# Kernel optimization log

Measured on AMD Instinct MI355X. Metric: run time of the kernel, lower is better.

## Reference

```python
import jax, jax.numpy as jnp
import numpy as np

GRID = 20            # grid_size -> n1 = 400 nodes
CTX = 64             # context_size
HID = 10 * CTX       # hidden_dim per module code
BATCH = 256
K_ITERS = 100        # Dykstra iterations approximating the exact QP solve
LEAKY_SLOPE = 0.1


def _grid_incidence(g):
    """Incidence matrix of g x g grid DAG with right/down edges (SPO benchmark)."""
    n1 = g * g
    edges = []
    for i in range(g):
        for j in range(g):
            u = i * g + j
            if j + 1 < g:
                edges.append((u, u + 1))   # right
            if i + 1 < g:
                edges.append((u, u + g))   # down
    n2 = len(edges)
    A = np.zeros((n1, n2), dtype=np.float32)
    for e, (u, v) in enumerate(edges):
        A[u, e] = 1.0    # flow leaves u
        A[v, e] = -1.0   # flow enters v
    b = np.zeros(n1, dtype=np.float32)
    b[0] = 1.0           # source
    b[-1] = -1.0         # sink
    return A, b


def setup_inputs() -> dict:
    key = jax.random.key(0)
    ks = jax.random.split(key, 5)
    A_np, b_np = _grid_incidence(GRID)
    n2 = A_np.shape[1]
    d = jax.random.normal(ks[0], (BATCH, CTX), dtype=jnp.float32)
    W1 = jax.random.normal(ks[1], (CTX, HID), dtype=jnp.float32) / np.sqrt(CTX)
    b1 = jax.random.normal(ks[2], (HID,), dtype=jnp.float32) * 0.01
    W2 = jax.random.normal(ks[3], (HID, n2), dtype=jnp.float32) / np.sqrt(HID)
    b2 = jax.random.normal(ks[4], (n2,), dtype=jnp.float32) * 0.01
    return {
        "d": d, "W1": W1, "b1": b1, "W2": W2, "b2": b2,
        "A": jnp.asarray(A_np), "b_eq": jnp.asarray(b_np),
    }


def _solve_qp(w, A, b_eq):
    """Batched min_x w'x + 0.5||x||^2 s.t. Ax=b, x>=0 == proj of -w onto the
    feasible set, via Dykstra alternating projections (affine set / orthant)."""
    M = jnp.linalg.pinv(A @ A.T)  # [n1, n1]; AA' is the grid Laplacian (rank n1-1)

    def proj_affine(x):           # x: [B, n2]
        resid = x @ A.T - b_eq    # [B, n1]
        return x - (resid @ M) @ A

    y0 = -w                       # point to project
    p0 = jnp.zeros_like(w)
    q0 = jnp.zeros_like(w)

    def step(carry, _):
        y, p, q = carry
        t = y + p
        yp = proj_affine(t)
        p = t - yp
        t2 = yp + q
        y = jnp.maximum(t2, 0.0)  # projection onto x >= 0
        q = t2 - y
        return (y, p, q), None

    (y, _, _), _ = jax.lax.scan(step, (y0, p0, q0), None, length=K_ITERS)
    return y


def reference(d, W1, b1, W2, b2, A, b_eq):
    h = d @ W1 + b1
    h = jnp.where(h > 0, h, LEAKY_SLOPE * h)   # LeakyReLU(0.1)
    w = h @ W2 + b2                            # predicted edge costs [B, n2]
    return _solve_qp(w, A, b_eq)               # training-mode output: QP solution
```

## Files before the change

### kernel.cpp

```cpp
#include <hip/hip_runtime.h>
#include <math.h>

#define G 20
#define N1 400
#define N2 760
#define CTXS 64
#define HID 640
#define NB 256
#define ITERS 100
#define PI_F 3.14159265358979323846f

__device__ __forceinline__ int eR(int i, int j) { return (i < 19) ? (39 * i + 2 * j) : (741 + j); }
__device__ __forceinline__ int eD(int i, int j) { return (j < 19) ? (39 * i + 2 * j + 1) : (39 * i + 38); }

#define LOAD_ROW20(dst, base) do {                                          \
    const float4* _rp = (const float4*)(base);                              \
    float4 _r0 = _rp[0], _r1 = _rp[1], _r2 = _rp[2], _r3 = _rp[3], _r4 = _rp[4]; \
    dst[0]=_r0.x; dst[1]=_r0.y; dst[2]=_r0.z; dst[3]=_r0.w;                 \
    dst[4]=_r1.x; dst[5]=_r1.y; dst[6]=_r1.z; dst[7]=_r1.w;                 \
    dst[8]=_r2.x; dst[9]=_r2.y; dst[10]=_r2.z; dst[11]=_r2.w;               \
    dst[12]=_r3.x; dst[13]=_r3.y; dst[14]=_r3.z; dst[15]=_r3.w;             \
    dst[16]=_r4.x; dst[17]=_r4.y; dst[18]=_r4.z; dst[19]=_r4.w; } while (0)

__global__ __launch_bounds__(256, 1) void spnet_kernel(
    const float* __restrict__ dmat, const float* __restrict__ W1,
    const float* __restrict__ b1v, const float* __restrict__ W2,
    const float* __restrict__ b2v, float* __restrict__ out)
{
  const int tid = threadIdx.x;
  const int bb  = blockIdx.x;

  __shared__ __align__(16) float sdrow[CTXS];
  __shared__ __align__(16) float sh[HID];
  __shared__ __align__(16) float st0[N2];
  __shared__ __align__(16) float sc1[N1];
  __shared__ __align__(16) float sc2T[N1];
  __shared__ __align__(16) float sd1[N1];
  __shared__ __align__(16) float szz[N1];
  __shared__ __align__(16) float tRsTbuf[21][G];
  __shared__ __align__(16) float tDsT[G][G];

  for (int t = tid; t < 21 * G; t += 256) ((float*)tRsTbuf)[t] = 0.f;
  for (int t = tid; t < N1; t += 256) ((float*)tDsT)[t] = 0.f;
  if (tid < CTXS) sdrow[tid] = dmat[bb * CTXS + tid];

  const bool isC = (tid < 200);
  const int c  = tid / 10;
  const int u  = tid % 10;
  const int k0 = 2 * u;

  float VA0[10], VA1[10], VC[20], S0, S1;
  {
    const float n0 = 0.22360679774997896f, nk = 0.31622776601683794f;
#pragma unroll
    for (int i = 0; i < 10; ++i) {
      VA0[i] = ((k0 == 0) ? n0 : nk) * cosf((float)(k0 * (2 * i + 1)) * (PI_F / 40.f));
      VA1[i] = nk * cosf((float)((k0 + 1) * (2 * i + 1)) * (PI_F / 40.f));
    }
#pragma unroll
    for (int k = 0; k < 20; ++k)
      VC[k] = ((k == 0) ? n0 : nk) * cosf((float)(k * (2 * u + 1)) * (PI_F / 40.f));
    float lc = 2.f - 2.f * cosf((float)c * (PI_F / 20.f));
    float l0 = 2.f - 2.f * cosf((float)k0 * (PI_F / 20.f));
    float l1 = 2.f - 2.f * cosf((float)(k0 + 1) * (PI_F / 20.f));
    S0 = (c == 0 && k0 == 0) ? 0.f : 1.f / (lc + l0);
    S1 = 1.f / (lc + l1);
  }

  __syncthreads();

  if (tid < HID / 4) {
    float4 acc = *(const float4*)(b1v + 4 * tid);
#pragma unroll 4
    for (int k = 0; k < CTXS; k += 4) {
      float4 h4 = *(const float4*)(sdrow + k);
      const float* wb = W1 + k * HID + 4 * tid;
      float4 w0 = *(const float4*)(wb);
      float4 w1 = *(const float4*)(wb + HID);
      float4 w2 = *(const float4*)(wb + 2 * HID);
      float4 w3 = *(const float4*)(wb + 3 * HID);
      acc.x = fmaf(h4.x, w0.x, acc.x); acc.y = fmaf(h4.x, w0.y, acc.y);
      acc.z = fmaf(h4.x, w0.z, acc.z); acc.w = fmaf(h4.x, w0.w, acc.w);
      acc.x = fmaf(h4.y, w1.x, acc.x); acc.y = fmaf(h4.y, w1.y, acc.y);
      acc.z = fmaf(h4.y, w1.z, acc.z); acc.w = fmaf(h4.y, w1.w, acc.w);
      acc.x = fmaf(h4.z, w2.x, acc.x); acc.y = fmaf(h4.z, w2.y, acc.y);
      acc.z = fmaf(h4.z, w2.z, acc.z); acc.w = fmaf(h4.z, w2.w, acc.w);
      acc.x = fmaf(h4.w, w3.x, acc.x); acc.y = fmaf(h4.w, w3.y, acc.y);
      acc.z = fmaf(h4.w, w3.z, acc.z); acc.w = fmaf(h4.w, w3.w, acc.w);
    }
    acc.x = acc.x > 0.f ? acc.x : 0.1f * acc.x;
    acc.y = acc.y > 0.f ? acc.y : 0.1f * acc.y;
    acc.z = acc.z > 0.f ? acc.z : 0.1f * acc.z;
    acc.w = acc.w > 0.f ? acc.w : 0.1f * acc.w;
    *(float4*)(sh + 4 * tid) = acc;
  }
  __syncthreads();

  if (tid < N2 / 4) {
    float4 acc = *(const float4*)(b2v + 4 * tid);
#pragma unroll 2
    for (int k = 0; k < HID; k += 4) {
      float4 h4 = *(const float4*)(sh + k);
      const float* wb = W2 + k * N2 + 4 * tid;
      float4 w0 = *(const float4*)(wb);
      float4 w1 = *(const float4*)(wb + N2);
      float4 w2 = *(const float4*)(wb + 2 * N2);
      float4 w3 = *(const float4*)(wb + 3 * N2);
      acc.x = fmaf(h4.x, w0.x, acc.x); acc.y = fmaf(h4.x, w0.y, acc.y);
      acc.z = fmaf(h4.x, w0.z, acc.z); acc.w = fmaf(h4.x, w0.w, acc.w);
      acc.x = fmaf(h4.y, w1.x, acc.x); acc.y = fmaf(h4.y, w1.y, acc.y);
      acc.z = fmaf(h4.y, w1.z, acc.z); acc.w = fmaf(h4.y, w1.w, acc.w);
      acc.x = fmaf(h4.z, w2.x, acc.x); acc.y = fmaf(h4.z, w2.y, acc.y);
      acc.z = fmaf(h4.z, w2.z, acc.z); acc.w = fmaf(h4.z, w2.w, acc.w);
      acc.x = fmaf(h4.w, w3.x, acc.x); acc.y = fmaf(h4.w, w3.y, acc.y);
      acc.z = fmaf(h4.w, w3.z, acc.z); acc.w = fmaf(h4.w, w3.w, acc.w);
    }
    float4 s; s.x = -acc.x; s.y = -acc.y; s.z = -acc.z; s.w = -acc.w;
    *(float4*)(st0 + 4 * tid) = s;
  }

  const int  di = tid / 5, dj4 = (tid % 5) * 4;
  const bool dAct = (tid < 100) && (di < 19);
  float dT[4], dQ[4], dY[4];
  const int  rid = tid - 128;
  const bool isR = (rid >= 0 && rid < 100);
  const int  ri = isR ? (rid / 5) : 0, rj4 = isR ? ((rid % 5) * 4) : 0;
  float rT[4], rQ[4], rY[4];
#pragma unroll
  for (int m = 0; m < 4; ++m) { dT[m]=0.f; dQ[m]=0.f; dY[m]=0.f; rT[m]=0.f; rQ[m]=0.f; rY[m]=0.f; }

  __syncthreads();

  if (dAct) {
#pragma unroll
    for (int m = 0; m < 4; ++m) {
      dT[m] = st0[eD(di, dj4 + m)];
      tDsT[dj4 + m][di + 1] = dT[m];
    }
  }
  if (isR) {
#pragma unroll
    for (int m = 0; m < 4; ++m) {
      int j = rj4 + m;
      rT[m] = (j < 19) ? st0[eR(ri, j)] : 0.f;
      tRsTbuf[j + 1][ri] = rT[m];
    }
  }
  __syncthreads();

  for (int it = 0; it < ITERS; ++it) {
    if (isC) {
      float cur[20]; LOAD_ROW20(cur, &tRsTbuf[c + 1][0]);
      float lf_[20]; LOAD_ROW20(lf_, &tRsTbuf[c][0]);
      float dn_[20]; LOAD_ROW20(dn_, &tDsT[c][0]);
      float d_[20];
#pragma unroll
      for (int x = 0; x < 20; ++x) {
        float oD = (x < 19) ? dn_[x + 1] : 0.f;
        d_[x] = ((cur[x] + oD) - lf_[x]) - dn_[x];
      }
      if (c == 0)  d_[0]  -= 1.f;
      if (c == 19) d_[19] += 1.f;
      float a0 = 0.f, a1 = 0.f;
#pragma unroll
      for (int i = 0; i < 10; ++i) {
        float e_ = d_[i] + d_[19 - i], o_ = d_[i] - d_[19 - i];
        a0 = fmaf(VA0[i], e_, a0);
        a1 = fmaf(VA1[i], o_, a1);
      }
      sc1[k0 * G + c] = a0;
      sc1[(k0 + 1) * G + c] = a1;
    }
    __syncthreads();

    if (isC) {
      float d_[20]; LOAD_ROW20(d_, sc1 + 20 * c);
      float a0 = 0.f, a1 = 0.f;
#pragma unroll
      for (int j = 0; j < 10; ++j) {
        float e_ = d_[j] + d_[19 - j], o_ = d_[j] - d_[19 - j];
        a0 = fmaf(VA0[j], e_, a0);
        a1 = fmaf(VA1[j], o_, a1);
      }
      sc2T[k0 * G + c] = a0 * S0;
      sc2T[(k0 + 1) * G + c] = a1 * S1;
    }
    __syncthreads();

    if (isC) {
      float d_[20]; LOAD_ROW20(d_, sc2T + 20 * c);
      float E = 0.f, O = 0.f;
#pragma unroll
      for (int m = 0; m < 10; ++m) {
        E = fmaf(VC[2 * m], d_[2 * m], E);
        O = fmaf(VC[2 * m + 1], d_[2 * m + 1], O);
      }
      sd1[u * G + c] = E + O;
      sd1[(19 - u) * G + c] = E - O;
    }
    __syncthreads();

    if (isC) {
      float d_[20]; LOAD_ROW20(d_, sd1 + 20 * c);
      float E = 0.f, O = 0.f;
#pragma unroll
      for (int m = 0; m < 10; ++m) {
        E = fmaf(VC[2 * m], d_[2 * m], E);
        O = fmaf(VC[2 * m + 1], d_[2 * m + 1], O);
      }
      szz[c * G + u] = E + O;
      szz[c * G + (19 - u)] = E - O;
    }
    __syncthreads();

    if (isR) {
      float4 z4 = *(const float4*)&szz[ri * G + rj4];
      float  zR = (rj4 < 16) ? szz[ri * G + rj4 + 4] : 0.f;
      float pn[4] = {z4.x - z4.y, z4.y - z4.z, z4.z - z4.w, z4.w - zR};
      if (rj4 == 16) pn[3] = 0.f;
#pragma unroll
      for (int m = 0; m < 4; ++m) {
        float t2 = rT[m] - pn[m] + rQ[m];
        float yn = fmaxf(t2, 0.f);
        rQ[m] = t2 - yn; rY[m] = yn; rT[m] = yn + pn[m];
        tRsTbuf[rj4 + m + 1][ri] = rT[m];
      }
    }
    if (dAct) {
      float4 z4 = *(const float4*)&szz[di * G + dj4];
      float4 zb = *(const float4*)&szz[(di + 1) * G + dj4];
      float pn[4] = {z4.x - zb.x, z4.y - zb.y, z4.z - zb.z, z4.w - zb.w};
#pragma unroll
      for (int m = 0; m < 4; ++m) {
        float t2 = dT[m] - pn[m] + dQ[m];
        float yn = fmaxf(t2, 0.f);
        dQ[m] = t2 - yn; dY[m] = yn; dT[m] = yn + pn[m];
        tDsT[dj4 + m][di + 1] = dT[m];
      }
    }
    __syncthreads();
  }

  float* mine = out + bb * N2;
  if (isR) {
#pragma unroll
    for (int m = 0; m < 4; ++m) {
      int j = rj4 + m;
      if (j < 19) mine[eR(ri, j)] = rY[m];
    }
  }
  if (dAct) {
#pragma unroll
    for (int m = 0; m < 4; ++m) mine[eD(di, dj4 + m)] = dY[m];
  }
}

extern "C" void kernel_launch(void* const* d_in, const int* in_sizes, int n_in,
                              void* d_out, int out_size, void* d_ws, size_t ws_size,
                              hipStream_t stream) {
  const float* d   = (const float*)d_in[0];
  const float* W1  = (const float*)d_in[1];
  const float* b1  = (const float*)d_in[2];
  const float* W2  = (const float*)d_in[3];
  const float* b2  = (const float*)d_in[4];
  float* out = (float*)d_out;
  spnet_kernel<<<NB, 256, 0, stream>>>(d, W1, b1, W2, b2, out);
}
```

Before: 214.4 us.

## Repartition DCT stages per wavefront to replace block barriers with intra-wave fences

Reassigns threads for the second-through-fourth transform stages and the Dykstra update so that each wavefront owns a contiguous slab of rows, with per-wave scratch buffers (scTw, szzw). Two of the five block-wide __syncthreads per iteration become compiler memory fences, relying on wavefront lockstep execution to order LDS traffic within a wave. This cuts barrier count per iteration from five to three, at the cost of extra per-wave redundant work and register use for a second set of DCT coefficients. Correctness depends on implicit wave-synchronous LDS ordering on 64-wide wavefronts.

```diff
diff --git a/kernel.cpp b/kernel.cpp
--- a/kernel.cpp
+++ b/kernel.cpp
@@ -22,6 +22,8 @@
     dst[12]=_r3.x; dst[13]=_r3.y; dst[14]=_r3.z; dst[15]=_r3.w;             \
     dst[16]=_r4.x; dst[17]=_r4.y; dst[18]=_r4.z; dst[19]=_r4.w; } while (0)
 
+#define FENCE() asm volatile("" ::: "memory")
+
 __global__ __launch_bounds__(256, 1) void spnet_kernel(
     const float* __restrict__ dmat, const float* __restrict__ W1,
     const float* __restrict__ b1v, const float* __restrict__ W2,
@@ -29,42 +31,66 @@
 {
   const int tid = threadIdx.x;
   const int bb  = blockIdx.x;
+  const int w   = tid >> 6;
+  const int ln  = tid & 63;
 
   __shared__ __align__(16) float sdrow[CTXS];
   __shared__ __align__(16) float sh[HID];
   __shared__ __align__(16) float st0[N2];
   __shared__ __align__(16) float sc1[N1];
-  __shared__ __align__(16) float sc2T[N1];
   __shared__ __align__(16) float sd1[N1];
-  __shared__ __align__(16) float szz[N1];
+  __shared__ __align__(16) float scTw[4][6][20];
+  __shared__ __align__(16) float szzw[4][6][24];
   __shared__ __align__(16) float tRsTbuf[21][G];
   __shared__ __align__(16) float tDsT[G][G];
 
   for (int t = tid; t < 21 * G; t += 256) ((float*)tRsTbuf)[t] = 0.f;
   for (int t = tid; t < N1; t += 256) ((float*)tDsT)[t] = 0.f;
+  for (int t = tid; t < 4 * 6 * 24; t += 256) ((float*)szzw)[t] = 0.f;
   if (tid < CTXS) sdrow[tid] = dmat[bb * CTXS + tid];
 
   const bool isC = (tid < 200);
-  const int c  = tid / 10;
-  const int u  = tid % 10;
-  const int k0 = 2 * u;
-
-  float VA0[10], VA1[10], VC[20], S0, S1;
+  const int cA = tid / 10;
+  const int uA = tid % 10;
+
+  const int UBbase = (w == 0 ? 0 : w == 1 ? 2 : w == 2 ? 5 : 7);
+  const int Lb     = (w == 0 ? 0 : w == 1 ? 4 : w == 2 ? 10 : 14);
+  const int uB = UBbase + ((ln / 20) < 3 ? (ln / 20) : 2);
+  const int cB = ln % 20;
+  const int uCD = ln % 10;
+  const int cC = 5 * w + ln / 10;
+  const int slotC = cC - Lb;
+
+  const int rD = 5 * w + ln / 10;
+  const bool dActD = (ln < 60) && (rD < 20);
+  const bool is_r = (ln < 25);
+  const int eidx = is_r ? ln : (ln - 25);
+  const int erow = 5 * w + eidx / 5;
+  const int ecol = (eidx % 5) * 4;
+  const bool eAct = (ln < 50) && (is_r || erow < 19);
+
+  float VA0A[10], VA1A[10];
+  float VA0B[10], VA1B[10];
+  float VC[20];
+  float S0B, S1B;
   {
     const float n0 = 0.22360679774997896f, nk = 0.31622776601683794f;
+    const int k0A = 2 * uA, k0B = 2 * uB;
 #pragma unroll
     for (int i = 0; i < 10; ++i) {
-      VA0[i] = ((k0 == 0) ? n0 : nk) * cosf((float)(k0 * (2 * i + 1)) * (PI_F / 40.f));
-      VA1[i] = nk * cosf((float)((k0 + 1) * (2 * i + 1)) * (PI_F / 40.f));
+      VA0A[i] = ((k0A == 0) ? n0 : nk) * cosf((float)(k0A * (2 * i + 1)) * (PI_F / 40.f));
+      VA1A[i] = nk * cosf((float)((k0A + 1) * (2 * i + 1)) * (PI_F / 40.f));
+      VA0B[i] = ((k0B == 0) ? n0 : nk) * cosf((float)(k0B * (2 * i + 1)) * (PI_F / 40.f));
+      VA1B[i] = nk * cosf((float)((k0B + 1) * (2 * i + 1)) * (PI_F / 40.f));
     }
 #pragma unroll
     for (int k = 0; k < 20; ++k)
-      VC[k] = ((k == 0) ? n0 : nk) * cosf((float)(k * (2 * u + 1)) * (PI_F / 40.f));
-    float lc = 2.f - 2.f * cosf((float)c * (PI_F / 20.f));
-    float l0 = 2.f - 2.f * cosf((float)k0 * (PI_F / 20.f));
-    float l1 = 2.f - 2.f * cosf((float)(k0 + 1) * (PI_F / 20.f));
-    S0 = (c == 0 && k0 == 0) ? 0.f : 1.f / (lc + l0);
-    S1 = 1.f / (lc + l1);
+      VC[k] = ((k == 0) ? n0 : nk) * cosf((float)(k * (2 * uCD + 1)) * (PI_F / 40.f));
+    float lcB = 2.f - 2.f * cosf((float)cB * (PI_F / 20.f));
+    float l0B = 2.f - 2.f * cosf((float)k0B * (PI_F / 20.f));
+    float l1B = 2.f - 2.f * cosf((float)(k0B + 1) * (PI_F / 20.f));
+    S0B = (cB == 0 && k0B == 0) ? 0.f : 1.f / (lcB + l0B);
+    S1B = 1.f / (lcB + l1B);
   }
 
   __syncthreads();
@@ -119,139 +145,122 @@
     *(float4*)(st0 + 4 * tid) = s;
   }
 
-  const int  di = tid / 5, dj4 = (tid % 5) * 4;
-  const bool dAct = (tid < 100) && (di < 19);
-  float dT[4], dQ[4], dY[4];
-  const int  rid = tid - 128;
-  const bool isR = (rid >= 0 && rid < 100);
-  const int  ri = isR ? (rid / 5) : 0, rj4 = isR ? ((rid % 5) * 4) : 0;
-  float rT[4], rQ[4], rY[4];
-#pragma unroll
-  for (int m = 0; m < 4; ++m) { dT[m]=0.f; dQ[m]=0.f; dY[m]=0.f; rT[m]=0.f; rQ[m]=0.f; rY[m]=0.f; }
-
-  __syncthreads();
-
-  if (dAct) {
+  float eT[4], eQ[4], eY[4];
+#pragma unroll
+  for (int m = 0; m < 4; ++m) { eT[m] = 0.f; eQ[m] = 0.f; eY[m] = 0.f; }
+
+  __syncthreads();
+
+  if (eAct) {
 #pragma unroll
     for (int m = 0; m < 4; ++m) {
-      dT[m] = st0[eD(di, dj4 + m)];
-      tDsT[dj4 + m][di + 1] = dT[m];
-    }
-  }
-  if (isR) {
-#pragma unroll
-    for (int m = 0; m < 4; ++m) {
-      int j = rj4 + m;
-      rT[m] = (j < 19) ? st0[eR(ri, j)] : 0.f;
-      tRsTbuf[j + 1][ri] = rT[m];
-    }
+      int j = ecol + m;
+      eT[m] = is_r ? ((j < 19) ? st0[eR(erow, j)] : 0.f) : st0[eD(erow, j)];
+    }
+    float* tb = is_r ? &tRsTbuf[1][0] : &tDsT[0][1];
+#pragma unroll
+    for (int m = 0; m < 4; ++m) tb[(ecol + m) * G + erow] = eT[m];
   }
   __syncthreads();
 
   for (int it = 0; it < ITERS; ++it) {
     if (isC) {
-      float cur[20]; LOAD_ROW20(cur, &tRsTbuf[c + 1][0]);
-      float lf_[20]; LOAD_ROW20(lf_, &tRsTbuf[c][0]);
-      float dn_[20]; LOAD_ROW20(dn_, &tDsT[c][0]);
+      float cur[20]; LOAD_ROW20(cur, &tRsTbuf[cA + 1][0]);
+      float lf_[20]; LOAD_ROW20(lf_, &tRsTbuf[cA][0]);
+      float dn_[20]; LOAD_ROW20(dn_, &tDsT[cA][0]);
       float d_[20];
 #pragma unroll
       for (int x = 0; x < 20; ++x) {
         float oD = (x < 19) ? dn_[x + 1] : 0.f;
         d_[x] = ((cur[x] + oD) - lf_[x]) - dn_[x];
       }
-      if (c == 0)  d_[0]  -= 1.f;
-      if (c == 19) d_[19] += 1.f;
+      if (cA == 0)  d_[0]  -= 1.f;
+      if (cA == 19) d_[19] += 1.f;
       float a0 = 0.f, a1 = 0.f;
 #pragma unroll
       for (int i = 0; i < 10; ++i) {
         float e_ = d_[i] + d_[19 - i], o_ = d_[i] - d_[19 - i];
-        a0 = fmaf(VA0[i], e_, a0);
-        a1 = fmaf(VA1[i], o_, a1);
-      }
-      sc1[k0 * G + c] = a0;
-      sc1[(k0 + 1) * G + c] = a1;
+        a0 = fmaf(VA0A[i], e_, a0);
+        a1 = fmaf(VA1A[i], o_, a1);
+      }
+      sc1[(2 * uA) * G + cA] = a0;
+      sc1[(2 * uA + 1) * G + cA] = a1;
     }
     __syncthreads();
 
-    if (isC) {
-      float d_[20]; LOAD_ROW20(d_, sc1 + 20 * c);
+    if (ln < 60) {
+      float d_[20]; LOAD_ROW20(d_, sc1 + 20 * cB);
       float a0 = 0.f, a1 = 0.f;
 #pragma unroll
       for (int j = 0; j < 10; ++j) {
         float e_ = d_[j] + d_[19 - j], o_ = d_[j] - d_[19 - j];
-        a0 = fmaf(VA0[j], e_, a0);
-        a1 = fmaf(VA1[j], o_, a1);
-      }
-      sc2T[k0 * G + c] = a0 * S0;
-      sc2T[(k0 + 1) * G + c] = a1 * S1;
-    }
-    __syncthreads();
-
-    if (isC) {
-      float d_[20]; LOAD_ROW20(d_, sc2T + 20 * c);
+        a0 = fmaf(VA0B[j], e_, a0);
+        a1 = fmaf(VA1B[j], o_, a1);
+      }
+      int sB0 = 2 * (ln / 20 < 3 ? ln / 20 : 2);
+      scTw[w][sB0][cB]     = a0 * S0B;
+      scTw[w][sB0 + 1][cB] = a1 * S1B;
+    }
+    FENCE();
+    if (ln < 50) {
+      float d_[20]; LOAD_ROW20(d_, &scTw[w][slotC][0]);
       float E = 0.f, O = 0.f;
 #pragma unroll
       for (int m = 0; m < 10; ++m) {
         E = fmaf(VC[2 * m], d_[2 * m], E);
         O = fmaf(VC[2 * m + 1], d_[2 * m + 1], O);
       }
-      sd1[u * G + c] = E + O;
-      sd1[(19 - u) * G + c] = E - O;
+      sd1[uCD * G + cC] = E + O;
+      sd1[(19 - uCD) * G + cC] = E - O;
     }
     __syncthreads();
 
-    if (isC) {
-      float d_[20]; LOAD_ROW20(d_, sd1 + 20 * c);
+    if (dActD) {
+      float d_[20]; LOAD_ROW20(d_, sd1 + 20 * rD);
       float E = 0.f, O = 0.f;
 #pragma unroll
       for (int m = 0; m < 10; ++m) {
         E = fmaf(VC[2 * m], d_[2 * m], E);
         O = fmaf(VC[2 * m + 1], d_[2 * m + 1], O);
       }
-      szz[c * G + u] = E + O;
-      szz[c * G + (19 - u)] = E - O;
+      szzw[w][ln / 10][uCD] = E + O;
+      szzw[w][ln / 10][19 - uCD] = E - O;
+    }
+    FENCE();
+    if (eAct) {
+      int slot = erow - 5 * w;
+      const float* zr = &szzw[w][slot][0];
+      float4 z4 = *(const float4*)(zr + ecol);
+      const float* p2 = is_r ? (zr + ecol + 4) : (&szzw[w][slot + 1][ecol]);
+      float4 v2 = *(const float4*)p2;
+      if (is_r) v2 = make_float4(z4.y, z4.z, z4.w, v2.x);
+      float pn[4] = {z4.x - v2.x, z4.y - v2.y, z4.z - v2.z, z4.w - v2.w};
+      if (is_r && ecol == 16) pn[3] = 0.f;
+#pragma unroll
+      for (int m = 0; m < 4; ++m) {
+        float t2 = eT[m] - pn[m] + eQ[m];
+        float yn = fmaxf(t2, 0.f);
+        eQ[m] = t2 - yn; eY[m] = yn; eT[m] = yn + pn[m];
+      }
+      float* tb = is_r ? &tRsTbuf[1][0] : &tDsT[0][1];
+#pragma unroll
+      for (int m = 0; m < 4; ++m) tb[(ecol + m) * G + erow] = eT[m];
     }
     __syncthreads();
-
-    if (isR) {
-      float4 z4 = *(const float4*)&szz[ri * G + rj4];
-      float  zR = (rj4 < 16) ? szz[ri * G + rj4 + 4] : 0.f;
-      float pn[4] = {z4.x - z4.y, z4.y - z4.z, z4.z - z4.w, z4.w - zR};
-      if (rj4 == 16) pn[3] = 0.f;
+  }
+
+  float* mine = out + bb * N2;
+  if (eAct) {
+    if (is_r) {
 #pragma unroll
       for (int m = 0; m < 4; ++m) {
-        float t2 = rT[m] - pn[m] + rQ[m];
-        float yn = fmaxf(t2, 0.f);
-        rQ[m] = t2 - yn; rY[m] = yn; rT[m] = yn + pn[m];
-        tRsTbuf[rj4 + m + 1][ri] = rT[m];
-      }
-    }
-    if (dAct) {
-      float4 z4 = *(const float4*)&szz[di * G + dj4];
-      float4 zb = *(const float4*)&szz[(di + 1) * G + dj4];
-      float pn[4] = {z4.x - zb.x, z4.y - zb.y, z4.z - zb.z, z4.w - zb.w};
-#pragma unroll
-      for (int m = 0; m < 4; ++m) {
-        float t2 = dT[m] - pn[m] + dQ[m];
-        float yn = fmaxf(t2, 0.f);
-        dQ[m] = t2 - yn; dY[m] = yn; dT[m] = yn + pn[m];
-        tDsT[dj4 + m][di + 1] = dT[m];
-      }
-    }
-    __syncthreads();
-  }
-
-  float* mine = out + bb * N2;
-  if (isR) {
-#pragma unroll
-    for (int m = 0; m < 4; ++m) {
-      int j = rj4 + m;
-      if (j < 19) mine[eR(ri, j)] = rY[m];
-    }
-  }
-  if (dAct) {
-#pragma unroll
-    for (int m = 0; m < 4; ++m) mine[eD(di, dj4 + m)] = dY[m];
+        int j = ecol + m;
+        if (j < 19) mine[eR(erow, j)] = eY[m];
+      }
+    } else {
+#pragma unroll
+      for (int m = 0; m < 4; ++m) mine[eD(erow, ecol + m)] = eY[m];
+    }
   }
 }
 
```

Result: no change. 212.6 us (-0.9%).
